# Kernel tuning notes

Measured on AMD Instinct MI355X. Metric: run time of the kernel, lower is better.

Reference implementation:

```python
import jax, jax.numpy as jnp
import numpy as np
from jax import lax

B, NBB, C, H, W = 32, 16, 1024, 22, 22
P = 3            # pooled output size (3x3)
SCALE = 1.0 / 16.0
EPS = 1e-5


def setup_inputs() -> dict:
    key = jax.random.key(0)
    ks = jax.random.split(key, 12)
    feat = jax.random.normal(ks[0], (B, C, H, W), jnp.float32)
    # bbox in xywh image coords, in-range for a 352x352 search region
    xy = jax.random.uniform(ks[1], (B, NBB, 2), jnp.float32, 0.0, 250.0)
    wh = jax.random.uniform(ks[2], (B, NBB, 2), jnp.float32, 16.0, 100.0)
    bbox = jnp.concatenate([xy, wh], axis=-1)
    conv_w = jax.random.normal(ks[3], (C, C, 3, 3), jnp.float32) * 0.01
    conv_b = jnp.zeros((C,), jnp.float32)
    bn_gamma = jnp.ones((C,), jnp.float32)
    bn_beta = jnp.zeros((C,), jnp.float32)
    bn_mean = jax.random.normal(ks[4], (C,), jnp.float32) * 0.1
    bn_var = jax.random.uniform(ks[5], (C,), jnp.float32, 0.5, 1.5)
    w1 = jax.random.normal(ks[6], (C // 2, C), jnp.float32) * 0.02
    b1 = jnp.zeros((C // 2,), jnp.float32)
    w2 = jax.random.normal(ks[7], (C // 2, C // 2), jnp.float32) * 0.02
    b2 = jnp.zeros((C // 2,), jnp.float32)
    w3 = jax.random.normal(ks[8], (512, C // 2), jnp.float32) * 0.02
    b3 = jnp.zeros((512,), jnp.float32)
    return dict(feat=feat, bbox=bbox, conv_w=conv_w, conv_b=conv_b,
                bn_gamma=bn_gamma, bn_beta=bn_beta, bn_mean=bn_mean, bn_var=bn_var,
                w1=w1, b1=b1, w2=w2, b2=b2, w3=w3, b3=b3)


def _hat_int(t):
    # Antiderivative of the bilinear hat h(u)=max(0,1-|u|), clipped to support.
    t = jnp.clip(t, -1.0, 1.0)
    return t + 0.5 - 0.5 * t * jnp.abs(t)


def _bin_weights(lo, bw, n):
    # lo, bw: [B, NBB].  Returns exact integral weights [B, NBB, P, n]:
    # W[b,r,p,i] = integral over bin p of hat(x - i) dx  (PrRoI closed form).
    p = jnp.arange(P, dtype=lo.dtype)
    xs = lo[..., None] + p * bw[..., None]          # [B,NBB,P] bin starts
    xe = xs + bw[..., None]                          # bin ends
    i = jnp.arange(n, dtype=lo.dtype)
    return _hat_int(xe[..., None] - i) - _hat_int(xs[..., None] - i)


def reference(feat, bbox, conv_w, conv_b, bn_gamma, bn_beta, bn_mean, bn_var,
              w1, b1, w2, b2, w3, b3):
    # --- PrRoI pooling (exact separable bilinear integral) ---
    x1 = bbox[..., 0] * SCALE
    y1 = bbox[..., 1] * SCALE
    x2 = (bbox[..., 0] + bbox[..., 2]) * SCALE
    y2 = (bbox[..., 1] + bbox[..., 3]) * SCALE
    bw = (x2 - x1) / P
    bh = (y2 - y1) / P
    Wx = _bin_weights(x1, bw, W)                     # [B,NBB,P,W]
    Wy = _bin_weights(y1, bh, H)                     # [B,NBB,P,H]
    pooled = jnp.einsum('bchw,bnqh,bnpw->bncqp', feat, Wy, Wx)  # [B,NBB,C,P,P]
    area = jnp.maximum(bw * bh, 0.0)[..., None, None, None]
    pooled = jnp.where(area > 0, pooled / jnp.maximum(area, 1e-12), 0.0)
    x = pooled.reshape(B * NBB, C, P, P)

    # --- conv_bn_relu: 3x3 conv, valid padding -> 1x1, BN (eval), ReLU ---
    x = lax.conv_general_dilated(x, conv_w, (1, 1), 'VALID',
                                 dimension_numbers=('NCHW', 'OIHW', 'NCHW'))
    x = x + conv_b[:, None, None]
    x = (x - bn_mean[:, None, None]) * (bn_gamma * lax.rsqrt(bn_var + EPS))[:, None, None]
    x = x + bn_beta[:, None, None]
    x = jax.nn.relu(x)

    # --- MLP head ---
    x = x.reshape(B * NBB, C)
    x = jax.nn.relu(x @ w1.T + b1)
    x = jax.nn.relu(x @ w2.T + b2)
    x = x @ w3.T + b3
    return x.reshape(B, NBB, 512)
```

## Files before the change

kernel.cpp:

```cpp
#include <hip/hip_runtime.h>
#include <hip/hip_bf16.h>

#define B_    32
#define NBB_  16
#define C_    1024
#define NROI  512
#define KCONV 9216
#define SCALE_ (1.0f/16.0f)
#define EPS_  1e-5f

using f32x4  = __attribute__((ext_vector_type(4))) float;
using bf16x8 = __attribute__((ext_vector_type(8))) short;

__device__ __forceinline__ unsigned f2bf(float f) {
  union { float f; unsigned u; } x; x.f = f;
  unsigned r = x.u + 0x7fffu + ((x.u >> 16) & 1u);
  return r >> 16;
}

__device__ __forceinline__ unsigned pk_bf16(float lo, float hi) {
  __hip_bfloat162 h = __float22bfloat162_rn(make_float2(lo, hi));
  return *reinterpret_cast<unsigned*>(&h);
}

__device__ __forceinline__ float hat_int(float t) {
  t = fminf(fmaxf(t, -1.f), 1.f);
  return t + 0.5f - 0.5f * t * fabsf(t);
}

__device__ __forceinline__ void glds16(const void* g, void* l) {
  __builtin_amdgcn_global_load_lds((const __attribute__((address_space(1))) void*)g,
                                   (__attribute__((address_space(3))) void*)l, 16, 0, 0);
}

__global__ __launch_bounds__(192) void prep_w2d(const float* __restrict__ bbox,
                                                unsigned short* __restrict__ W2d) {
  __shared__ float wyS[16*66], wxS[16*66];
  int b = blockIdx.x, tid = threadIdx.x;
  for (int t = tid; t < 352; t += 192) {
    int n = t / 22, i = t - n * 22;
    float4 bb = ((const float4*)bbox)[b*16 + n];
    float x1 = bb.x * SCALE_, y1 = bb.y * SCALE_;
    float x2 = (bb.x + bb.z) * SCALE_, y2 = (bb.y + bb.w) * SCALE_;
    float bw = (x2 - x1) / 3.f, bh = (y2 - y1) / 3.f;
    float area = fmaxf(bw * bh, 0.f);
    float inv = area > 0.f ? 1.f / fmaxf(area, 1e-12f) : 0.f;
    float fi = (float)i;
#pragma unroll
    for (int q = 0; q < 3; ++q) {
      float sy = y1 + q * bh;
      wyS[n*66 + q*22 + i] = hat_int(sy + bh - fi) - hat_int(sy - fi);
      float sx = x1 + q * bw;
      wxS[n*66 + q*22 + i] = (hat_int(sx + bw - fi) - hat_int(sx - fi)) * inv;
    }
  }
  __syncthreads();
  if (tid < 144) {
    int n = tid / 9, qp = tid - n*9, q = qp / 3, p = qp - q*3;
    const float* wyp = wyS + n*66 + q*22;
    const float* wxp = wxS + n*66 + p*22;
    unsigned short* out = W2d + ((size_t)b*144 + tid) * 512;
    for (int h = 0; h < 22; ++h) {
      float yv = wyp[h];
      int kb = h * 22;
#pragma unroll
      for (int w = 0; w < 22; w += 2)
        *(unsigned*)&out[kb + w] = pk_bf16(yv * wxp[w], yv * wxp[w+1]);
    }
#pragma unroll
    for (int k = 484; k < 512; k += 2) *(unsigned*)&out[k] = 0u;
  }
}

__global__ __launch_bounds__(256) void cvt_bf16(const float* __restrict__ src,
                                                unsigned short* __restrict__ dst, int n8) {
  int i = blockIdx.x * 256 + threadIdx.x;
  if (i >= n8) return;
  float4 a = ((const float4*)src)[2*i];
  float4 b = ((const float4*)src)[2*i + 1];
  uint4 pk;
  pk.x = pk_bf16(a.x, a.y); pk.y = pk_bf16(a.z, a.w);
  pk.z = pk_bf16(b.x, b.y); pk.w = pk_bf16(b.z, b.w);
  ((uint4*)dst)[i] = pk;
}

__global__ __launch_bounds__(256) void convw_t(const float* __restrict__ cw,
                                               unsigned short* __restrict__ out) {
  __shared__ unsigned short T[9][1028];
  int o = blockIdx.x, tid = threadIdx.x;
  const float4* src = (const float4*)(cw + (size_t)o * 9216);
#pragma unroll
  for (int it = 0; it < 9; ++it) {
    int i = tid + it * 256;
    float4 v = src[i];
    int e = i * 4;
    {
      int c = e / 9, qp = e - c * 9;
      T[qp][c] = (unsigned short)f2bf(v.x);
    }
    { int ee = e+1; int c = ee / 9, qp = ee - c * 9; T[qp][c] = (unsigned short)f2bf(v.y); }
    { int ee = e+2; int c = ee / 9, qp = ee - c * 9; T[qp][c] = (unsigned short)f2bf(v.z); }
    { int ee = e+3; int c = ee / 9, qp = ee - c * 9; T[qp][c] = (unsigned short)f2bf(v.w); }
  }
  __syncthreads();
  unsigned short* dst = out + (size_t)o * 9216;
#pragma unroll
  for (int qp = 0; qp < 9; ++qp) {
    uint2 w = *(const uint2*)&T[qp][tid * 4];
    ((uint2*)(dst + qp * 1024))[tid] = w;
  }
}

__global__ __launch_bounds__(384) void pool_gemm(const float* __restrict__ feat,
                                                 const unsigned short* __restrict__ W2d,
                                                 unsigned short* __restrict__ X) {
  __shared__ __align__(16) unsigned short Bs[64 * 72];
  int tid = threadIdx.x;
  int nch = blockIdx.x, b = blockIdx.y;
  int lane = tid & 63, wid = tid >> 6;
  int wm = wid >> 1, wn = wid & 1;
  int l15 = lane & 15, kg = lane >> 4;
  const unsigned short* w2b = W2d + (size_t)b * 144 * 512;
  const float* fb = feat + ((size_t)b * C_ + (size_t)nch * 64) * 484;
  f32x4 acc[3][2] = {};

  int c0 = tid >> 4,        f40 = tid & 15;
  int i1 = tid + 384;  int c1 = i1 >> 4, f41 = i1 & 15;
  int i2 = tid + 768;  bool has2 = i2 < 1024; int c2 = i2 >> 4, f42 = i2 & 15;
  float4 bR0, bR1, bR2;

#define LOADB(s) do { \
    bR0 = (((s) < 7 || f40 <= 8) ? *(const float4*)(fb + (size_t)c0*484 + (s)*64 + f40*4) : make_float4(0,0,0,0)); \
    bR1 = (((s) < 7 || f41 <= 8) ? *(const float4*)(fb + (size_t)c1*484 + (s)*64 + f41*4) : make_float4(0,0,0,0)); \
    if (has2) bR2 = (((s) < 7 || f42 <= 8) ? *(const float4*)(fb + (size_t)c2*484 + (s)*64 + f42*4) : make_float4(0,0,0,0)); \
  } while (0)

  LOADB(0);
#pragma unroll
  for (int s = 0; s < 8; ++s) {
    __syncthreads();
    {
      uint2 p0; p0.x = pk_bf16(bR0.x, bR0.y); p0.y = pk_bf16(bR0.z, bR0.w);
      *(uint2*)&Bs[c0*72 + f40*4] = p0;
      uint2 p1; p1.x = pk_bf16(bR1.x, bR1.y); p1.y = pk_bf16(bR1.z, bR1.w);
      *(uint2*)&Bs[c1*72 + f41*4] = p1;
      if (has2) {
        uint2 p2; p2.x = pk_bf16(bR2.x, bR2.y); p2.y = pk_bf16(bR2.z, bR2.w);
        *(uint2*)&Bs[c2*72 + f42*4] = p2;
      }
    }
    if (s < 7) LOADB(s + 1);
    __syncthreads();

    bf16x8 af[3][2], bf[2][2];
#pragma unroll
    for (int fm = 0; fm < 3; ++fm)
#pragma unroll
      for (int kk = 0; kk < 2; ++kk)
        af[fm][kk] = *(const bf16x8*)(w2b + (size_t)(wm*48 + fm*16 + l15) * 512 + s*64 + kk*32 + kg*8);
#pragma unroll
    for (int fn = 0; fn < 2; ++fn)
#pragma unroll
      for (int kk = 0; kk < 2; ++kk)
        bf[fn][kk] = *(const bf16x8*)&Bs[(wn*32 + fn*16 + l15) * 72 + kk*32 + kg*8];
#pragma unroll
    for (int fm = 0; fm < 3; ++fm)
#pragma unroll
      for (int fn = 0; fn < 2; ++fn) {
        acc[fm][fn] = __builtin_amdgcn_mfma_f32_16x16x32_bf16(af[fm][0], bf[fn][0], acc[fm][fn], 0, 0, 0);
        acc[fm][fn] = __builtin_amdgcn_mfma_f32_16x16x32_bf16(af[fm][1], bf[fn][1], acc[fm][fn], 0, 0, 0);
      }
  }
#undef LOADB

#pragma unroll
  for (int fm = 0; fm < 3; ++fm)
#pragma unroll
    for (int r = 0; r < 4; ++r) {
      int m = wm*48 + fm*16 + kg*4 + r;
      int n = m / 9, qp = m - n*9;
      size_t base = ((size_t)(b*16 + n)) * KCONV + (size_t)qp * 1024 + (size_t)nch * 64;
#pragma unroll
      for (int fn = 0; fn < 2; ++fn)
        X[base + wn*32 + fn*16 + l15] = (unsigned short)f2bf(acc[fm][fn][r]);
    }
}

__global__ __launch_bounds__(256) void gemm128(const unsigned short* __restrict__ A,
                                               const unsigned short* __restrict__ Bm,
                                               float* __restrict__ Cp,
                                               int M, int N, int K, int kChunk) {
  __shared__ __align__(16) unsigned short As[2][4096];
  __shared__ __align__(16) unsigned short Bs[2][4096];
  int tid = threadIdx.x;
  int lane = tid & 63, wid = tid >> 6;
  int wm = wid >> 1, wn = wid & 1;
  int l15 = lane & 15, kg = lane >> 4;
  int nt = blockIdx.x, mt = blockIdx.y, z = blockIdx.z;
  int kbeg = z * kChunk;
  int steps = kChunk / 32;

  int row0 = tid >> 2, row1 = 64 + row0;
  int slot = tid & 3;
  int s0 = slot ^ ((row0 >> 1) & 3);
  int s1 = slot ^ ((row1 >> 1) & 3);
  const unsigned short* ga0 = A  + (size_t)(mt*128 + row0) * K + kbeg + s0*8;
  const unsigned short* ga1 = A  + (size_t)(mt*128 + row1) * K + kbeg + s1*8;
  const unsigned short* gb0 = Bm + (size_t)(nt*128 + row0) * K + kbeg + s0*8;
  const unsigned short* gb1 = Bm + (size_t)(nt*128 + row1) * K + kbeg + s1*8;
  int wbyte = wid * 1024;

  f32x4 acc[4][4] = {};
  int cur = 0;

#define ISSUE(buf, s) do { int ko = (s) * 32; \
    glds16(ga0 + ko, (char*)&As[(buf)][0] + wbyte); \
    glds16(ga1 + ko, (char*)&As[(buf)][0] + 4096 + wbyte); \
    glds16(gb0 + ko, (char*)&Bs[(buf)][0] + wbyte); \
    glds16(gb1 + ko, (char*)&Bs[(buf)][0] + 4096 + wbyte); } while (0)

  ISSUE(0, 0);
  for (int s = 0; s < steps; ++s) {
    __syncthreads();
    if (s + 1 < steps) ISSUE(cur ^ 1, s + 1);
    bf16x8 af[4], bfr[4];
#pragma unroll
    for (int fm = 0; fm < 4; ++fm) {
      int fr = wm*64 + fm*16 + l15;
      af[fm] = *(const bf16x8*)&As[cur][fr*32 + ((kg ^ ((fr >> 1) & 3)) << 3)];
    }
#pragma unroll
    for (int fn = 0; fn < 4; ++fn) {
      int fr = wn*64 + fn*16 + l15;
      bfr[fn] = *(const bf16x8*)&Bs[cur][fr*32 + ((kg ^ ((fr >> 1) & 3)) << 3)];
    }
#pragma unroll
    for (int fm = 0; fm < 4; ++fm)
#pragma unroll
      for (int fn = 0; fn < 4; ++fn)
        acc[fm][fn] = __builtin_amdgcn_mfma_f32_16x16x32_bf16(af[fm], bfr[fn], acc[fm][fn], 0, 0, 0);
    cur ^= 1;
  }
#undef ISSUE

  float* cp = Cp + ((size_t)z * M + (size_t)mt * 128) * N + (size_t)nt * 128;
#pragma unroll
  for (int fm = 0; fm < 4; ++fm)
#pragma unroll
    for (int fn = 0; fn < 4; ++fn)
#pragma unroll
      for (int r = 0; r < 4; ++r) {
        int row = wm*64 + fm*16 + kg*4 + r;
        int col = wn*64 + fn*16 + l15;
        cp[(size_t)row * N + col] = acc[fm][fn][r];
      }
}

__global__ __launch_bounds__(256) void gemm_nt(const unsigned short* __restrict__ A,
                                               const unsigned short* __restrict__ Bm,
                                               float* __restrict__ Cp,
                                               int M, int N, int K, int kChunk) {
  __shared__ __align__(16) unsigned short As[64][40];
  __shared__ __align__(16) unsigned short Bs[64][40];
  int tid = threadIdx.x;
  int lane = tid & 63, wid = tid >> 6;
  int wm = wid >> 1, wn = wid & 1;
  int l15 = lane & 15, kg = lane >> 4;
  int nt = blockIdx.x, mt = blockIdx.y, z = blockIdx.z;
  int kbeg = z * kChunk;
  int kend = kbeg + kChunk; if (kend > K) kend = K;
  int srow = tid >> 2, sseg = tid & 3;
  const unsigned short* aG = A  + (size_t)(mt*64 + srow) * K + sseg * 8;
  const unsigned short* bG = Bm + (size_t)(nt*64 + srow) * K + sseg * 8;
  f32x4 acc[2][2] = {};

  for (int k0 = kbeg; k0 < kend; k0 += 32) {
    uint4 av = *(const uint4*)(aG + k0);
    uint4 bv = *(const uint4*)(bG + k0);
    __syncthreads();
    *(uint4*)&As[srow][sseg*8] = av;
    *(uint4*)&Bs[srow][sseg*8] = bv;
    __syncthreads();
    bf16x8 a0 = *(const bf16x8*)&As[wm*32 +      l15][kg*8];
    bf16x8 a1 = *(const bf16x8*)&As[wm*32 + 16 + l15][kg*8];
    bf16x8 b0 = *(const bf16x8*)&Bs[wn*32 +      l15][kg*8];
    bf16x8 b1 = *(const bf16x8*)&Bs[wn*32 + 16 + l15][kg*8];
    acc[0][0] = __builtin_amdgcn_mfma_f32_16x16x32_bf16(a0, b0, acc[0][0], 0, 0, 0);
    acc[0][1] = __builtin_amdgcn_mfma_f32_16x16x32_bf16(a0, b1, acc[0][1], 0, 0, 0);
    acc[1][0] = __builtin_amdgcn_mfma_f32_16x16x32_bf16(a1, b0, acc[1][0], 0, 0, 0);
    acc[1][1] = __builtin_amdgcn_mfma_f32_16x16x32_bf16(a1, b1, acc[1][1], 0, 0, 0);
  }

  float* cp = Cp + ((size_t)z * M + (size_t)mt * 64) * N + (size_t)nt * 64;
#pragma unroll
  for (int fm = 0; fm < 2; ++fm)
#pragma unroll
    for (int fn = 0; fn < 2; ++fn)
#pragma unroll
      for (int r = 0; r < 4; ++r) {
        int row = wm*32 + fm*16 + kg*4 + r;
        int col = wn*32 + fn*16 + l15;
        cp[(size_t)row * N + col] = acc[fm][fn][r];
      }
}

template<int MODE>
__global__ __launch_bounds__(256) void epi(const float* __restrict__ Cp, int SK, int MN4, int N,
                                           const float* __restrict__ bias,
                                           const float* __restrict__ g,
                                           const float* __restrict__ be,
                                           const float* __restrict__ mu,
                                           const float* __restrict__ var,
                                           unsigned short* __restrict__ outb,
                                           float* __restrict__ outf) {
  int i = blockIdx.x * 256 + threadIdx.x;
  if (i >= MN4) return;
  float4 s = ((const float4*)Cp)[i];
  for (int z = 1; z < SK; ++z) {
    float4 t = ((const float4*)Cp)[(size_t)z * MN4 + i];
    s.x += t.x; s.y += t.y; s.z += t.z; s.w += t.w;
  }
  int n0 = (i * 4) % N;
  float v[4] = {s.x, s.y, s.z, s.w};
  if (MODE == 0) {
    float o[4];
#pragma unroll
    for (int j = 0; j < 4; ++j) {
      int n = n0 + j;
      float sc = g[n] * rsqrtf(var[n] + EPS_);
      o[j] = fmaxf((v[j] + bias[n] - mu[n]) * sc + be[n], 0.f);
    }
    uint2 pk; pk.x = pk_bf16(o[0], o[1]); pk.y = pk_bf16(o[2], o[3]);
    *(uint2*)&outb[(size_t)i * 4] = pk;
  } else if (MODE == 1) {
    uint2 pk;
    pk.x = pk_bf16(fmaxf(v[0] + bias[n0], 0.f),     fmaxf(v[1] + bias[n0+1], 0.f));
    pk.y = pk_bf16(fmaxf(v[2] + bias[n0+2], 0.f),   fmaxf(v[3] + bias[n0+3], 0.f));
    *(uint2*)&outb[(size_t)i * 4] = pk;
  } else {
    float4 o;
    o.x = v[0] + bias[n0];     o.y = v[1] + bias[n0 + 1];
    o.z = v[2] + bias[n0 + 2]; o.w = v[3] + bias[n0 + 3];
    ((float4*)outf)[i] = o;
  }
}

extern "C" void kernel_launch(void* const* d_in, const int* in_sizes, int n_in,
                              void* d_out, int out_size, void* d_ws, size_t ws_size,
                              hipStream_t stream) {
  const float* feat   = (const float*)d_in[0];
  const float* bbox   = (const float*)d_in[1];
  const float* conv_w = (const float*)d_in[2];
  const float* conv_b = (const float*)d_in[3];
  const float* gamma  = (const float*)d_in[4];
  const float* beta   = (const float*)d_in[5];
  const float* mean   = (const float*)d_in[6];
  const float* var    = (const float*)d_in[7];
  const float* w1     = (const float*)d_in[8];
  const float* b1     = (const float*)d_in[9];
  const float* w2     = (const float*)d_in[10];
  const float* b2     = (const float*)d_in[11];
  const float* w3     = (const float*)d_in[12];
  const float* b3     = (const float*)d_in[13];

  char* ws = (char*)d_ws;
  unsigned short* W2d = (unsigned short*)(ws);
  unsigned short* Xb  = (unsigned short*)(ws + 4718592);
  unsigned short* Wfb = (unsigned short*)(ws + 14155776);
  unsigned short* w1b = (unsigned short*)(ws + 33030144);
  unsigned short* w2b = (unsigned short*)(ws + 34078720);
  unsigned short* w3b = (unsigned short*)(ws + 34603008);
  float*          part= (float*)(ws + 35127296);
  unsigned short* H0  = (unsigned short*)(ws + 51904512);
  unsigned short* H1  = (unsigned short*)(ws + 52953088);
  unsigned short* H2  = (unsigned short*)(ws + 53477376);

  prep_w2d<<<32, 192, 0, stream>>>(bbox, W2d);
  convw_t<<<1024, 256, 0, stream>>>(conv_w, Wfb);
  cvt_bf16<<<(65536 + 255) / 256, 256, 0, stream>>>(w1, w1b, 65536);
  cvt_bf16<<<(32768 + 255) / 256, 256, 0, stream>>>(w2, w2b, 32768);
  cvt_bf16<<<(32768 + 255) / 256, 256, 0, stream>>>(w3, w3b, 32768);

  pool_gemm<<<dim3(16, 32), 384, 0, stream>>>(feat, W2d, Xb);

  gemm128<<<dim3(8, 4, 8), 256, 0, stream>>>(Xb, Wfb, part, 512, 1024, 9216, 1152);
  epi<0><<<(131072 + 255) / 256, 256, 0, stream>>>(part, 8, 131072, 1024,
      conv_b, gamma, beta, mean, var, H0, nullptr);

  gemm_nt<<<dim3(8, 8, 4), 256, 0, stream>>>(H0, w1b, part, 512, 512, 1024, 256);
  epi<1><<<(65536 + 255) / 256, 256, 0, stream>>>(part, 4, 65536, 512,
      b1, nullptr, nullptr, nullptr, nullptr, H1, nullptr);

  gemm_nt<<<dim3(8, 8, 4), 256, 0, stream>>>(H1, w2b, part, 512, 512, 512, 128);
  epi<1><<<(65536 + 255) / 256, 256, 0, stream>>>(part, 4, 65536, 512,
      b2, nullptr, nullptr, nullptr, nullptr, H2, nullptr);

  gemm_nt<<<dim3(8, 8, 4), 256, 0, stream>>>(H2, w3b, part, 512, 512, 512, 128);
  epi<2><<<(65536 + 255) / 256, 256, 0, stream>>>(part, 4, 65536, 512,
      b3, nullptr, nullptr, nullptr, nullptr, nullptr, (float*)d_out);
}
```

Before: 126.8 us.

## Pre-convert features to padded bf16 and pipeline pool GEMM with async LDS loads

Adds a separate pass that converts the feature map to bf16, padded from 484 to 512 elements per channel. The pooling GEMM then loads both operands straight into double-buffered, XOR-swizzled LDS through glds16, with a 128-channel tile per block. The three weight-conversion launches are merged into one, and the workspace layout is reordered so the partial-sum buffer aliases the early scratch. This moves the per-tile fp32-to-bf16 conversion out of the GEMM loop and overlaps global loads with MFMA work. The cost is an extra kernel that writes and re-reads an 8M-element bf16 feature copy.

```diff
diff --git a/kernel.cpp b/kernel.cpp
--- a/kernel.cpp
+++ b/kernel.cpp
@@ -72,16 +72,21 @@
   }
 }
 
-__global__ __launch_bounds__(256) void cvt_bf16(const float* __restrict__ src,
-                                                unsigned short* __restrict__ dst, int n8) {
+__global__ __launch_bounds__(256) void cvt3_bf16(const float* __restrict__ w1, const float* __restrict__ w2,
+                                                 const float* __restrict__ w3,
+                                                 unsigned short* __restrict__ o1, unsigned short* __restrict__ o2,
+                                                 unsigned short* __restrict__ o3) {
   int i = blockIdx.x * 256 + threadIdx.x;
-  if (i >= n8) return;
-  float4 a = ((const float4*)src)[2*i];
-  float4 b = ((const float4*)src)[2*i + 1];
+  const float* src; unsigned short* dst; int g;
+  if (i < 65536)      { src = w1; dst = o1; g = i; }
+  else if (i < 98304) { src = w2; dst = o2; g = i - 65536; }
+  else                { src = w3; dst = o3; g = i - 98304; }
+  float4 a = ((const float4*)src)[2*g];
+  float4 b = ((const float4*)src)[2*g + 1];
   uint4 pk;
   pk.x = pk_bf16(a.x, a.y); pk.y = pk_bf16(a.z, a.w);
   pk.z = pk_bf16(b.x, b.y); pk.w = pk_bf16(b.z, b.w);
-  ((uint4*)dst)[i] = pk;
+  ((uint4*)dst)[g] = pk;
 }
 
 __global__ __launch_bounds__(256) void convw_t(const float* __restrict__ cw,
@@ -94,13 +99,10 @@
     int i = tid + it * 256;
     float4 v = src[i];
     int e = i * 4;
-    {
-      int c = e / 9, qp = e - c * 9;
-      T[qp][c] = (unsigned short)f2bf(v.x);
-    }
-    { int ee = e+1; int c = ee / 9, qp = ee - c * 9; T[qp][c] = (unsigned short)f2bf(v.y); }
-    { int ee = e+2; int c = ee / 9, qp = ee - c * 9; T[qp][c] = (unsigned short)f2bf(v.z); }
-    { int ee = e+3; int c = ee / 9, qp = ee - c * 9; T[qp][c] = (unsigned short)f2bf(v.w); }
+    { int c = e / 9,     qp = e - c*9;             T[qp][c] = (unsigned short)f2bf(v.x); }
+    { int ee = e+1; int c = ee / 9, qp = ee - c*9; T[qp][c] = (unsigned short)f2bf(v.y); }
+    { int ee = e+2; int c = ee / 9, qp = ee - c*9; T[qp][c] = (unsigned short)f2bf(v.z); }
+    { int ee = e+3; int c = ee / 9, qp = ee - c*9; T[qp][c] = (unsigned short)f2bf(v.w); }
   }
   __syncthreads();
   unsigned short* dst = out + (size_t)o * 9216;
@@ -111,67 +113,82 @@
   }
 }
 
-__global__ __launch_bounds__(384) void pool_gemm(const float* __restrict__ feat,
-                                                 const unsigned short* __restrict__ W2d,
+__global__ __launch_bounds__(256) void cvt_feat(const float* __restrict__ feat,
+                                                unsigned short* __restrict__ featB) {
+  int blk = blockIdx.x;
+  int tid = threadIdx.x;
+  const float4* src = (const float4*)(feat + (size_t)blk * 16 * 484);
+  unsigned short* dstB = featB + (size_t)blk * 16 * 512;
+#pragma unroll
+  for (int it = 0; it < 8; ++it) {
+    int j = tid + it * 256;
+    if (j < 1936) {
+      float4 v = src[j];
+      int lin = j * 4;
+      int c = lin / 484, w = lin - c * 484;
+      uint2 pk;
+      pk.x = pk_bf16(v.x, v.y); pk.y = pk_bf16(v.z, v.w);
+      *(uint2*)&dstB[(size_t)c * 512 + w] = pk;
+    }
+  }
+  if (tid < 112) {
+    int c = tid / 7, ws = tid - c * 7;
+    uint2 z; z.x = 0u; z.y = 0u;
+    *(uint2*)&dstB[(size_t)c * 512 + 484 + ws * 4] = z;
+  }
+}
+
+__global__ __launch_bounds__(384) void pool_gemm(const unsigned short* __restrict__ W2d,
+                                                 const unsigned short* __restrict__ featB,
                                                  unsigned short* __restrict__ X) {
-  __shared__ __align__(16) unsigned short Bs[64 * 72];
+  __shared__ __align__(16) unsigned short As[2][4608];
+  __shared__ __align__(16) unsigned short Bs[2][4096];
   int tid = threadIdx.x;
-  int nch = blockIdx.x, b = blockIdx.y;
+  int nt = blockIdx.x, b = blockIdx.y;
   int lane = tid & 63, wid = tid >> 6;
   int wm = wid >> 1, wn = wid & 1;
   int l15 = lane & 15, kg = lane >> 4;
-  const unsigned short* w2b = W2d + (size_t)b * 144 * 512;
-  const float* fb = feat + ((size_t)b * C_ + (size_t)nch * 64) * 484;
-  f32x4 acc[3][2] = {};
-
-  int c0 = tid >> 4,        f40 = tid & 15;
-  int i1 = tid + 384;  int c1 = i1 >> 4, f41 = i1 & 15;
-  int i2 = tid + 768;  bool has2 = i2 < 1024; int c2 = i2 >> 4, f42 = i2 & 15;
-  float4 bR0, bR1, bR2;
-
-#define LOADB(s) do { \
-    bR0 = (((s) < 7 || f40 <= 8) ? *(const float4*)(fb + (size_t)c0*484 + (s)*64 + f40*4) : make_float4(0,0,0,0)); \
-    bR1 = (((s) < 7 || f41 <= 8) ? *(const float4*)(fb + (size_t)c1*484 + (s)*64 + f41*4) : make_float4(0,0,0,0)); \
-    if (has2) bR2 = (((s) < 7 || f42 <= 8) ? *(const float4*)(fb + (size_t)c2*484 + (s)*64 + f42*4) : make_float4(0,0,0,0)); \
-  } while (0)
-
-  LOADB(0);
-#pragma unroll
-  for (int s = 0; s < 8; ++s) {
+  const unsigned short* aBase = W2d  + (size_t)b * 144 * 512;
+  const unsigned short* bBase = featB + ((size_t)b * 1024 + (size_t)nt * 128) * 512;
+  f32x4 acc[3][4] = {};
+
+#define ISSUEP(buf, s) do { int k0_ = (s) * 32; \
+    _Pragma("unroll") for (int ii = 0; ii < 3; ++ii) { \
+      int sb = ii*384 + wid*64; \
+      if (sb < 1088) { \
+        int slot = sb + lane; \
+        if (sb < 576) { \
+          int row = slot >> 2, seg = (slot & 3) ^ ((row >> 1) & 3); \
+          glds16(aBase + (size_t)row*512 + k0_ + seg*8, (char*)&As[(buf)][0] + sb*16); \
+        } else { \
+          int s2 = slot - 576; int row = s2 >> 2, seg = (s2 & 3) ^ ((row >> 1) & 3); \
+          glds16(bBase + (size_t)row*512 + k0_ + seg*8, (char*)&Bs[(buf)][0] + (sb-576)*16); \
+        } } } } while (0)
+
+  ISSUEP(0, 0);
+  int cur = 0;
+  for (int s = 0; s < 16; ++s) {
     __syncthreads();
-    {
-      uint2 p0; p0.x = pk_bf16(bR0.x, bR0.y); p0.y = pk_bf16(bR0.z, bR0.w);
-      *(uint2*)&Bs[c0*72 + f40*4] = p0;
-      uint2 p1; p1.x = pk_bf16(bR1.x, bR1.y); p1.y = pk_bf16(bR1.z, bR1.w);
-      *(uint2*)&Bs[c1*72 + f41*4] = p1;
-      if (has2) {
-        uint2 p2; p2.x = pk_bf16(bR2.x, bR2.y); p2.y = pk_bf16(bR2.z, bR2.w);
-        *(uint2*)&Bs[c2*72 + f42*4] = p2;
-      }
-    }
-    if (s < 7) LOADB(s + 1);
-    __syncthreads();
-
-    bf16x8 af[3][2], bf[2][2];
+    if (s < 15) ISSUEP(cur ^ 1, s + 1);
+    bf16x8 af[3], bfr[4];
+#pragma unroll
+    for (int fm = 0; fm < 3; ++fm) {
+      int r = wm*48 + fm*16 + l15;
+      af[fm] = *(const bf16x8*)&As[cur][r*32 + ((kg ^ ((r >> 1) & 3)) << 3)];
+    }
+#pragma unroll
+    for (int fn = 0; fn < 4; ++fn) {
+      int r = wn*64 + fn*16 + l15;
+      bfr[fn] = *(const bf16x8*)&Bs[cur][r*32 + ((kg ^ ((r >> 1) & 3)) << 3)];
+    }
 #pragma unroll
     for (int fm = 0; fm < 3; ++fm)
 #pragma unroll
-      for (int kk = 0; kk < 2; ++kk)
-        af[fm][kk] = *(const bf16x8*)(w2b + (size_t)(wm*48 + fm*16 + l15) * 512 + s*64 + kk*32 + kg*8);
-#pragma unroll
-    for (int fn = 0; fn < 2; ++fn)
-#pragma unroll
-      for (int kk = 0; kk < 2; ++kk)
-        bf[fn][kk] = *(const bf16x8*)&Bs[(wn*32 + fn*16 + l15) * 72 + kk*32 + kg*8];
-#pragma unroll
-    for (int fm = 0; fm < 3; ++fm)
-#pragma unroll
-      for (int fn = 0; fn < 2; ++fn) {
-        acc[fm][fn] = __builtin_amdgcn_mfma_f32_16x16x32_bf16(af[fm][0], bf[fn][0], acc[fm][fn], 0, 0, 0);
-        acc[fm][fn] = __builtin_amdgcn_mfma_f32_16x16x32_bf16(af[fm][1], bf[fn][1], acc[fm][fn], 0, 0, 0);
-      }
-  }
-#undef LOADB
+      for (int fn = 0; fn < 4; ++fn)
+        acc[fm][fn] = __builtin_amdgcn_mfma_f32_16x16x32_bf16(af[fm], bfr[fn], acc[fm][fn], 0, 0, 0);
+    cur ^= 1;
+  }
+#undef ISSUEP
 
 #pragma unroll
   for (int fm = 0; fm < 3; ++fm)
@@ -179,10 +196,10 @@
     for (int r = 0; r < 4; ++r) {
       int m = wm*48 + fm*16 + kg*4 + r;
       int n = m / 9, qp = m - n*9;
-      size_t base = ((size_t)(b*16 + n)) * KCONV + (size_t)qp * 1024 + (size_t)nch * 64;
-#pragma unroll
-      for (int fn = 0; fn < 2; ++fn)
-        X[base + wn*32 + fn*16 + l15] = (unsigned short)f2bf(acc[fm][fn][r]);
+      size_t base = ((size_t)(b*16 + n)) * KCONV + (size_t)qp * 1024 + (size_t)nt * 128;
+#pragma unroll
+      for (int fn = 0; fn < 4; ++fn)
+        X[base + wn*64 + fn*16 + l15] = (unsigned short)f2bf(acc[fm][fn][r]);
     }
 }
 
@@ -334,8 +351,8 @@
     *(uint2*)&outb[(size_t)i * 4] = pk;
   } else if (MODE == 1) {
     uint2 pk;
-    pk.x = pk_bf16(fmaxf(v[0] + bias[n0], 0.f),     fmaxf(v[1] + bias[n0+1], 0.f));
-    pk.y = pk_bf16(fmaxf(v[2] + bias[n0+2], 0.f),   fmaxf(v[3] + bias[n0+3], 0.f));
+    pk.x = pk_bf16(fmaxf(v[0] + bias[n0], 0.f),   fmaxf(v[1] + bias[n0+1], 0.f));
+    pk.y = pk_bf16(fmaxf(v[2] + bias[n0+2], 0.f), fmaxf(v[3] + bias[n0+3], 0.f));
     *(uint2*)&outb[(size_t)i * 4] = pk;
   } else {
     float4 o;
@@ -364,24 +381,24 @@
   const float* b3     = (const float*)d_in[13];
 
   char* ws = (char*)d_ws;
-  unsigned short* W2d = (unsigned short*)(ws);
-  unsigned short* Xb  = (unsigned short*)(ws + 4718592);
-  unsigned short* Wfb = (unsigned short*)(ws + 14155776);
-  unsigned short* w1b = (unsigned short*)(ws + 33030144);
-  unsigned short* w2b = (unsigned short*)(ws + 34078720);
-  unsigned short* w3b = (unsigned short*)(ws + 34603008);
-  float*          part= (float*)(ws + 35127296);
-  unsigned short* H0  = (unsigned short*)(ws + 51904512);
-  unsigned short* H1  = (unsigned short*)(ws + 52953088);
-  unsigned short* H2  = (unsigned short*)(ws + 53477376);
+  unsigned short* W2d  = (unsigned short*)(ws);
+  unsigned short* featB= (unsigned short*)(ws + 4718592);
+  float*          part = (float*)(ws);
+  unsigned short* H0   = (unsigned short*)(ws + 16777216);
+  unsigned short* H1   = (unsigned short*)(ws + 17825792);
+  unsigned short* H2   = (unsigned short*)(ws + 18350080);
+  unsigned short* Xb   = (unsigned short*)(ws + 38273024);
+  unsigned short* Wfb  = (unsigned short*)(ws + 47710208);
+  unsigned short* w1b  = (unsigned short*)(ws + 66584576);
+  unsigned short* w2b  = (unsigned short*)(ws + 67633152);
+  unsigned short* w3b  = (unsigned short*)(ws + 68157440);
 
   prep_w2d<<<32, 192, 0, stream>>>(bbox, W2d);
   convw_t<<<1024, 256, 0, stream>>>(conv_w, Wfb);
-  cvt_bf16<<<(65536 + 255) / 256, 256, 0, stream>>>(w1, w1b, 65536);
-  cvt_bf16<<<(32768 + 255) / 256, 256, 0, stream>>>(w2, w2b, 32768);
-  cvt_bf16<<<(32768 + 255) / 256, 256, 0, stream>>>(w3, w3b, 32768);
-
-  pool_gemm<<<dim3(16, 32), 384, 0, stream>>>(feat, W2d, Xb);
+  cvt3_bf16<<<512, 256, 0, stream>>>(w1, w2, w3, w1b, w2b, w3b);
+  cvt_feat<<<2048, 256, 0, stream>>>(feat, featB);
+
+  pool_gemm<<<dim3(8, 32), 384, 0, stream>>>(W2d, featB, Xb);
 
   gemm128<<<dim3(8, 4, 8), 256, 0, stream>>>(Xb, Wfb, part, 512, 1024, 9216, 1152);
   epi<0><<<(131072 + 255) / 256, 256, 0, stream>>>(part, 8, 131072, 1024,
```

After: 130.5 us. 2.9% more time.

## Merge prep kernels into one launch and fuse MLP GEMM epilogues without split-K

Applied to the files above, without the earlier changes.

Five preprocessing kernels (bbox weight build, conv weight transpose, three bf16 conversions) are combined into a single launch that dispatches on block index. The three MLP GEMMs drop split-K and the separate reduction/epilogue kernels; each now runs over the full K and applies bias, ReLU and bf16 conversion directly in its store loop. This removes about eight kernel launches and the fp32 partial-sum round trips through global memory. In exchange, each MLP GEMM runs only 64 blocks, which leaves most of the GPU idle and lengthens the serial K loop.

```diff
diff --git a/kernel.cpp b/kernel.cpp
--- a/kernel.cpp
+++ b/kernel.cpp
@@ -33,81 +33,87 @@
                                    (__attribute__((address_space(3))) void*)l, 16, 0, 0);
 }
 
-__global__ __launch_bounds__(192) void prep_w2d(const float* __restrict__ bbox,
-                                                unsigned short* __restrict__ W2d) {
-  __shared__ float wyS[16*66], wxS[16*66];
-  int b = blockIdx.x, tid = threadIdx.x;
-  for (int t = tid; t < 352; t += 192) {
-    int n = t / 22, i = t - n * 22;
-    float4 bb = ((const float4*)bbox)[b*16 + n];
-    float x1 = bb.x * SCALE_, y1 = bb.y * SCALE_;
-    float x2 = (bb.x + bb.z) * SCALE_, y2 = (bb.y + bb.w) * SCALE_;
-    float bw = (x2 - x1) / 3.f, bh = (y2 - y1) / 3.f;
-    float area = fmaxf(bw * bh, 0.f);
-    float inv = area > 0.f ? 1.f / fmaxf(area, 1e-12f) : 0.f;
-    float fi = (float)i;
-#pragma unroll
-    for (int q = 0; q < 3; ++q) {
-      float sy = y1 + q * bh;
-      wyS[n*66 + q*22 + i] = hat_int(sy + bh - fi) - hat_int(sy - fi);
-      float sx = x1 + q * bw;
-      wxS[n*66 + q*22 + i] = (hat_int(sx + bw - fi) - hat_int(sx - fi)) * inv;
-    }
-  }
-  __syncthreads();
-  if (tid < 144) {
-    int n = tid / 9, qp = tid - n*9, q = qp / 3, p = qp - q*3;
-    const float* wyp = wyS + n*66 + q*22;
-    const float* wxp = wxS + n*66 + p*22;
-    unsigned short* out = W2d + ((size_t)b*144 + tid) * 512;
-    for (int h = 0; h < 22; ++h) {
-      float yv = wyp[h];
-      int kb = h * 22;
-#pragma unroll
-      for (int w = 0; w < 22; w += 2)
-        *(unsigned*)&out[kb + w] = pk_bf16(yv * wxp[w], yv * wxp[w+1]);
-    }
-#pragma unroll
-    for (int k = 484; k < 512; k += 2) *(unsigned*)&out[k] = 0u;
-  }
-}
-
-__global__ __launch_bounds__(256) void cvt_bf16(const float* __restrict__ src,
-                                                unsigned short* __restrict__ dst, int n8) {
-  int i = blockIdx.x * 256 + threadIdx.x;
-  if (i >= n8) return;
-  float4 a = ((const float4*)src)[2*i];
-  float4 b = ((const float4*)src)[2*i + 1];
-  uint4 pk;
-  pk.x = pk_bf16(a.x, a.y); pk.y = pk_bf16(a.z, a.w);
-  pk.z = pk_bf16(b.x, b.y); pk.w = pk_bf16(b.z, b.w);
-  ((uint4*)dst)[i] = pk;
-}
-
-__global__ __launch_bounds__(256) void convw_t(const float* __restrict__ cw,
-                                               unsigned short* __restrict__ out) {
-  __shared__ unsigned short T[9][1028];
-  int o = blockIdx.x, tid = threadIdx.x;
-  const float4* src = (const float4*)(cw + (size_t)o * 9216);
-#pragma unroll
-  for (int it = 0; it < 9; ++it) {
-    int i = tid + it * 256;
-    float4 v = src[i];
-    int e = i * 4;
-    {
-      int c = e / 9, qp = e - c * 9;
-      T[qp][c] = (unsigned short)f2bf(v.x);
-    }
-    { int ee = e+1; int c = ee / 9, qp = ee - c * 9; T[qp][c] = (unsigned short)f2bf(v.y); }
-    { int ee = e+2; int c = ee / 9, qp = ee - c * 9; T[qp][c] = (unsigned short)f2bf(v.z); }
-    { int ee = e+3; int c = ee / 9, qp = ee - c * 9; T[qp][c] = (unsigned short)f2bf(v.w); }
-  }
-  __syncthreads();
-  unsigned short* dst = out + (size_t)o * 9216;
-#pragma unroll
-  for (int qp = 0; qp < 9; ++qp) {
-    uint2 w = *(const uint2*)&T[qp][tid * 4];
-    ((uint2*)(dst + qp * 1024))[tid] = w;
+__global__ __launch_bounds__(256) void prep_all(
+    const float* __restrict__ bbox, const float* __restrict__ conv_w,
+    const float* __restrict__ w1, const float* __restrict__ w2, const float* __restrict__ w3,
+    unsigned short* __restrict__ W2d, unsigned short* __restrict__ Wfb,
+    unsigned short* __restrict__ o1, unsigned short* __restrict__ o2,
+    unsigned short* __restrict__ o3)
+{
+  __shared__ __align__(16) char psm[18504];
+  int tid = threadIdx.x;
+  int bx = blockIdx.x;
+
+  if (bx < 32) {
+    int b = bx;
+    float* wyS = (float*)psm;
+    float* wxS = wyS + 1056;
+    for (int t = tid; t < 352; t += 256) {
+      int n = t / 22, i = t - n * 22;
+      float4 bb = ((const float4*)bbox)[b*16 + n];
+      float x1 = bb.x * SCALE_, y1 = bb.y * SCALE_;
+      float x2 = (bb.x + bb.z) * SCALE_, y2 = (bb.y + bb.w) * SCALE_;
+      float bw = (x2 - x1) / 3.f, bh = (y2 - y1) / 3.f;
+      float area = fmaxf(bw * bh, 0.f);
+      float inv = area > 0.f ? 1.f / fmaxf(area, 1e-12f) : 0.f;
+      float fi = (float)i;
+#pragma unroll
+      for (int q = 0; q < 3; ++q) {
+        float sy = y1 + q * bh;
+        wyS[n*66 + q*22 + i] = hat_int(sy + bh - fi) - hat_int(sy - fi);
+        float sx = x1 + q * bw;
+        wxS[n*66 + q*22 + i] = (hat_int(sx + bw - fi) - hat_int(sx - fi)) * inv;
+      }
+    }
+    __syncthreads();
+    if (tid < 144) {
+      int n = tid / 9, qp = tid - n*9, q = qp / 3, p = qp - q*3;
+      const float* wyp = wyS + n*66 + q*22;
+      const float* wxp = wxS + n*66 + p*22;
+      unsigned short* out = W2d + ((size_t)b*144 + tid) * 512;
+      for (int h = 0; h < 22; ++h) {
+        float yv = wyp[h];
+        int kb = h * 22;
+#pragma unroll
+        for (int w = 0; w < 22; w += 2)
+          *(unsigned*)&out[kb + w] = pk_bf16(yv * wxp[w], yv * wxp[w+1]);
+      }
+#pragma unroll
+      for (int k = 484; k < 512; k += 2) *(unsigned*)&out[k] = 0u;
+    }
+  } else if (bx < 1056) {
+    int o = bx - 32;
+    unsigned short (*T)[1028] = (unsigned short(*)[1028])psm;
+    const float4* src = (const float4*)(conv_w + (size_t)o * 9216);
+#pragma unroll
+    for (int it = 0; it < 9; ++it) {
+      int i = tid + it * 256;
+      float4 v = src[i];
+      int e = i * 4;
+      { int c = e / 9,     qp = e - c*9;             T[qp][c] = (unsigned short)f2bf(v.x); }
+      { int ee = e+1; int c = ee / 9, qp = ee - c*9; T[qp][c] = (unsigned short)f2bf(v.y); }
+      { int ee = e+2; int c = ee / 9, qp = ee - c*9; T[qp][c] = (unsigned short)f2bf(v.z); }
+      { int ee = e+3; int c = ee / 9, qp = ee - c*9; T[qp][c] = (unsigned short)f2bf(v.w); }
+    }
+    __syncthreads();
+    unsigned short* dst = Wfb + (size_t)o * 9216;
+#pragma unroll
+    for (int qp = 0; qp < 9; ++qp) {
+      uint2 w = *(const uint2*)&T[qp][tid * 4];
+      ((uint2*)(dst + qp * 1024))[tid] = w;
+    }
+  } else {
+    int i = (bx - 1056) * 256 + tid;
+    const float* src; unsigned short* dst; int g;
+    if (i < 65536)      { src = w1; dst = o1; g = i; }
+    else if (i < 98304) { src = w2; dst = o2; g = i - 65536; }
+    else                { src = w3; dst = o3; g = i - 98304; }
+    float4 a = ((const float4*)src)[2*g];
+    float4 b = ((const float4*)src)[2*g + 1];
+    uint4 pk;
+    pk.x = pk_bf16(a.x, a.y); pk.y = pk_bf16(a.z, a.w);
+    pk.z = pk_bf16(b.x, b.y); pk.w = pk_bf16(b.z, b.w);
+    ((uint4*)dst)[g] = pk;
   }
 }
 
@@ -256,25 +262,53 @@
       }
 }
 
-__global__ __launch_bounds__(256) void gemm_nt(const unsigned short* __restrict__ A,
-                                               const unsigned short* __restrict__ Bm,
-                                               float* __restrict__ Cp,
-                                               int M, int N, int K, int kChunk) {
+__global__ __launch_bounds__(256) void epi0(const float* __restrict__ Cp, int SK, int MN4,
+                                            const float* __restrict__ bias,
+                                            const float* __restrict__ g,
+                                            const float* __restrict__ be,
+                                            const float* __restrict__ mu,
+                                            const float* __restrict__ var,
+                                            unsigned short* __restrict__ outb) {
+  int i = blockIdx.x * 256 + threadIdx.x;
+  if (i >= MN4) return;
+  float4 s = ((const float4*)Cp)[i];
+  for (int z = 1; z < SK; ++z) {
+    float4 t = ((const float4*)Cp)[(size_t)z * MN4 + i];
+    s.x += t.x; s.y += t.y; s.z += t.z; s.w += t.w;
+  }
+  int n0 = (i * 4) & 1023;
+  float v[4] = {s.x, s.y, s.z, s.w};
+  float o[4];
+#pragma unroll
+  for (int j = 0; j < 4; ++j) {
+    int n = n0 + j;
+    float sc = g[n] * rsqrtf(var[n] + EPS_);
+    o[j] = fmaxf((v[j] + bias[n] - mu[n]) * sc + be[n], 0.f);
+  }
+  uint2 pk; pk.x = pk_bf16(o[0], o[1]); pk.y = pk_bf16(o[2], o[3]);
+  *(uint2*)&outb[(size_t)i * 4] = pk;
+}
+
+template<int MODE>
+__global__ __launch_bounds__(256) void gemm_full(const unsigned short* __restrict__ A,
+                                                 const unsigned short* __restrict__ Bm,
+                                                 int K,
+                                                 const float* __restrict__ bias,
+                                                 unsigned short* __restrict__ outb,
+                                                 float* __restrict__ outf) {
   __shared__ __align__(16) unsigned short As[64][40];
   __shared__ __align__(16) unsigned short Bs[64][40];
   int tid = threadIdx.x;
   int lane = tid & 63, wid = tid >> 6;
   int wm = wid >> 1, wn = wid & 1;
   int l15 = lane & 15, kg = lane >> 4;
-  int nt = blockIdx.x, mt = blockIdx.y, z = blockIdx.z;
-  int kbeg = z * kChunk;
-  int kend = kbeg + kChunk; if (kend > K) kend = K;
+  int nt = blockIdx.x, mt = blockIdx.y;
   int srow = tid >> 2, sseg = tid & 3;
   const unsigned short* aG = A  + (size_t)(mt*64 + srow) * K + sseg * 8;
   const unsigned short* bG = Bm + (size_t)(nt*64 + srow) * K + sseg * 8;
   f32x4 acc[2][2] = {};
 
-  for (int k0 = kbeg; k0 < kend; k0 += 32) {
+  for (int k0 = 0; k0 < K; k0 += 32) {
     uint4 av = *(const uint4*)(aG + k0);
     uint4 bv = *(const uint4*)(bG + k0);
     __syncthreads();
@@ -291,58 +325,20 @@
     acc[1][1] = __builtin_amdgcn_mfma_f32_16x16x32_bf16(a1, b1, acc[1][1], 0, 0, 0);
   }
 
-  float* cp = Cp + ((size_t)z * M + (size_t)mt * 64) * N + (size_t)nt * 64;
 #pragma unroll
   for (int fm = 0; fm < 2; ++fm)
 #pragma unroll
     for (int fn = 0; fn < 2; ++fn)
 #pragma unroll
       for (int r = 0; r < 4; ++r) {
-        int row = wm*32 + fm*16 + kg*4 + r;
-        int col = wn*32 + fn*16 + l15;
-        cp[(size_t)row * N + col] = acc[fm][fn][r];
-      }
-}
-
-template<int MODE>
-__global__ __launch_bounds__(256) void epi(const float* __restrict__ Cp, int SK, int MN4, int N,
-                                           const float* __restrict__ bias,
-                                           const float* __restrict__ g,
-                                           const float* __restrict__ be,
-                                           const float* __restrict__ mu,
-                                           const float* __restrict__ var,
-                                           unsigned short* __restrict__ outb,
-                                           float* __restrict__ outf) {
-  int i = blockIdx.x * 256 + threadIdx.x;
-  if (i >= MN4) return;
-  float4 s = ((const float4*)Cp)[i];
-  for (int z = 1; z < SK; ++z) {
-    float4 t = ((const float4*)Cp)[(size_t)z * MN4 + i];
-    s.x += t.x; s.y += t.y; s.z += t.z; s.w += t.w;
-  }
-  int n0 = (i * 4) % N;
-  float v[4] = {s.x, s.y, s.z, s.w};
-  if (MODE == 0) {
-    float o[4];
-#pragma unroll
-    for (int j = 0; j < 4; ++j) {
-      int n = n0 + j;
-      float sc = g[n] * rsqrtf(var[n] + EPS_);
-      o[j] = fmaxf((v[j] + bias[n] - mu[n]) * sc + be[n], 0.f);
-    }
-    uint2 pk; pk.x = pk_bf16(o[0], o[1]); pk.y = pk_bf16(o[2], o[3]);
-    *(uint2*)&outb[(size_t)i * 4] = pk;
-  } else if (MODE == 1) {
-    uint2 pk;
-    pk.x = pk_bf16(fmaxf(v[0] + bias[n0], 0.f),     fmaxf(v[1] + bias[n0+1], 0.f));
-    pk.y = pk_bf16(fmaxf(v[2] + bias[n0+2], 0.f),   fmaxf(v[3] + bias[n0+3], 0.f));
-    *(uint2*)&outb[(size_t)i * 4] = pk;
-  } else {
-    float4 o;
-    o.x = v[0] + bias[n0];     o.y = v[1] + bias[n0 + 1];
-    o.z = v[2] + bias[n0 + 2]; o.w = v[3] + bias[n0 + 3];
-    ((float4*)outf)[i] = o;
-  }
+        int grow = mt*64 + wm*32 + fm*16 + kg*4 + r;
+        int gcol = nt*64 + wn*32 + fn*16 + l15;
+        float v = acc[fm][fn][r] + bias[gcol];
+        if (MODE == 1)
+          outb[(size_t)grow * 512 + gcol] = (unsigned short)f2bf(fmaxf(v, 0.f));
+        else
+          outf[(size_t)grow * 512 + gcol] = v;
+      }
 }
 
 extern "C" void kernel_launch(void* const* d_in, const int* in_sizes, int n_in,
@@ -375,27 +371,14 @@
   unsigned short* H1  = (unsigned short*)(ws + 52953088);
   unsigned short* H2  = (unsigned short*)(ws + 53477376);
 
-  prep_w2d<<<32, 192, 0, stream>>>(bbox, W2d);
-  convw_t<<<1024, 256, 0, stream>>>(conv_w, Wfb);
-  cvt_bf16<<<(65536 + 255) / 256, 256, 0, stream>>>(w1, w1b, 65536);
-  cvt_bf16<<<(32768 + 255) / 256, 256, 0, stream>>>(w2, w2b, 32768);
-  cvt_bf16<<<(32768 + 255) / 256, 256, 0, stream>>>(w3, w3b, 32768);
+  prep_all<<<1568, 256, 0, stream>>>(bbox, conv_w, w1, w2, w3, W2d, Wfb, w1b, w2b, w3b);
 
   pool_gemm<<<dim3(16, 32), 384, 0, stream>>>(feat, W2d, Xb);
 
   gemm128<<<dim3(8, 4, 8), 256, 0, stream>>>(Xb, Wfb, part, 512, 1024, 9216, 1152);
-  epi<0><<<(131072 + 255) / 256, 256, 0, stream>>>(part, 8, 131072, 1024,
-      conv_b, gamma, beta, mean, var, H0, nullptr);
-
-  gemm_nt<<<dim3(8, 8, 4), 256, 0, stream>>>(H0, w1b, part, 512, 512, 1024, 256);
-  epi<1><<<(65536 + 255) / 256, 256, 0, stream>>>(part, 4, 65536, 512,
-      b1, nullptr, nullptr, nullptr, nullptr, H1, nullptr);
-
-  gemm_nt<<<dim3(8, 8, 4), 256, 0, stream>>>(H1, w2b, part, 512, 512, 512, 128);
-  epi<1><<<(65536 + 255) / 256, 256, 0, stream>>>(part, 4, 65536, 512,
-      b2, nullptr, nullptr, nullptr, nullptr, H2, nullptr);
-
-  gemm_nt<<<dim3(8, 8, 4), 256, 0, stream>>>(H2, w3b, part, 512, 512, 512, 128);
-  epi<2><<<(65536 + 255) / 256, 256, 0, stream>>>(part, 4, 65536, 512,
-      b3, nullptr, nullptr, nullptr, nullptr, nullptr, (float*)d_out);
-}
+  epi0<<<512, 256, 0, stream>>>(part, 8, 131072, conv_b, gamma, beta, mean, var, H0);
+
+  gemm_full<1><<<dim3(8, 8), 256, 0, stream>>>(H0, w1b, 1024, b1, H1, nullptr);
+  gemm_full<1><<<dim3(8, 8), 256, 0, stream>>>(H1, w2b, 512,  b2, H2, nullptr);
+  gemm_full<2><<<dim3(8, 8), 256, 0, stream>>>(H2, w3b, 512,  b3, nullptr, (float*)d_out);
+}
```

After: 124.4 us. Within noise of the previous version (-1.9%).
